# Kernel tuning notes

Hardware: AMD Instinct MI355X
Metric: run time of the kernel (lower is better)

The kernel has to match this reference:

```python
import jax, jax.numpy as jnp
import numpy as np

IB = 8; WB = 8; ABMVM = 8; ABNM = 8; N_MSB = 4; NL = 0.0  # noise_level=0 -> deterministic
B = 4096; IN = 1024; H = 1024

sg = jax.lax.stop_gradient

def quant_raw(x, bits, r):
    step = 2.0 ** (bits - 1)
    xs = jnp.clip(x / r, -1.0 + 1.0 / step, 1.0 - 1.0 / step)
    return jnp.round(xs * step) / step * r

def quant_ste(x, bits, r):
    # straight-through: value = quantized, grad = identity wrt x, no grad to r
    return x + sg(quant_raw(x, bits, r) - x)

def pact(x, a):
    # sign(x)*0.5*(|x| - ||x|-a| + a) == clamp(x, -a, a), kept literal for fidelity
    return jnp.sign(x) * 0.5 * (jnp.abs(x) - jnp.abs(jnp.abs(x) - a) + a)

def bitsplit(x, bits, n_msb):
    # symmetric bit-splitting; STE backward: each y_i has identity grad wrt x
    ste = x - sg(x)
    xv = sg(x)
    beta = 1.0
    ys = []
    for _ in range(n_msb):
        y = quant_raw(xv / beta, bits, 1.0)
        xv = xv - y * beta
        ys.append(y + ste)
        beta = beta / 2.0
    betas = jnp.asarray([1.0 / (2.0 ** i) for i in range(n_msb)], dtype=x.dtype)
    return jnp.stack(ys), betas  # [n_msb, B, D], [n_msb]

def custom_mm(inp, w, b, key):
    # forward: inp @ (quant(clamp(w)) + noise) + quant(b) + noise
    # backward (torch custom): grads use RAW w/b -> STE via out_lin path
    kw, kb = jax.random.split(key)
    n = inp.shape[0]
    noise_w = jax.random.normal(kw, (n, w.shape[1], w.shape[2]), dtype=w.dtype) * NL
    noise_b = jax.random.normal(kb, (n, 1, b.shape[2]), dtype=b.dtype) * NL
    wq = quant_raw(jnp.clip(w, -1.0, 1.0), WB, 1.0)
    bq = quant_raw(b, WB, 1.0)
    out_val = jnp.einsum('nbi,nio->nbo', inp, wq + noise_w) + (bq + noise_b)
    out_lin = jnp.einsum('nbi,io->nbo', inp, w[0]) + b
    return out_lin + sg(out_val - out_lin)

def _cell(input, hx, cx, weight_ih, weight_hh, bias_ih, bias_hh,
          a1, a3, a4, a5, a6, a7, a8, a9, a10, a11):
    k1, k2 = jax.random.split(jax.random.key(42))
    ys, betas = bitsplit(pact(input, a1) / a1, IB, N_MSB)
    out_q = quant_ste(custom_mm(ys, weight_ih, bias_ih, k1), ABMVM, 1.0)
    part1 = (betas[:, None, None] * out_q).sum(0) * a1          # [B, 4H]
    ys, betas = bitsplit(pact(hx, a11) / a11, IB, N_MSB)
    out_q = quant_ste(custom_mm(ys, weight_hh, bias_hh, k2), ABMVM, 1.0)
    part2 = (betas[:, None, None] * out_q).sum(0) * a11
    gates = part1 + part2
    i, j, f, o = jnp.split(gates, 4, axis=1)
    fg = quant_ste(pact(jax.nn.sigmoid(f), a3), ABNM, a3)
    ig = quant_ste(pact(jax.nn.sigmoid(i), a4), ABNM, a4)
    act = quant_ste(pact(jnp.tanh(j), a5), ABNM, a5)
    og = quant_ste(pact(jax.nn.sigmoid(o), a6), ABNM, a6)
    gc = quant_ste(pact(cx * fg, a7), ABNM, a7)
    ai = quant_ste(pact(ig * act, a8), ABNM, a8)
    new_c = quant_ste(pact(gc + ai, a9), ABNM, a9)
    ac = quant_ste(pact(jnp.tanh(new_c), a10), ABNM, a10)
    new_h = quant_ste(pact(ac * og, a11), ABNM, a11)
    return jnp.stack([new_h, new_c])  # [2, B, H]

def setup_inputs() -> dict:
    key = jax.random.key(0)
    ks = jax.random.split(key, 7)
    return {
        'input': jax.random.normal(ks[0], (B, IN), dtype=jnp.float32),
        'hx': jax.random.normal(ks[1], (B, H), dtype=jnp.float32),
        'cx': jax.random.normal(ks[2], (B, H), dtype=jnp.float32),
        'weight_ih': jax.random.normal(ks[3], (1, IN, 4 * H), dtype=jnp.float32) * 0.05,
        'weight_hh': jax.random.normal(ks[4], (1, H, 4 * H), dtype=jnp.float32) * 0.05,
        'bias_ih': jax.random.normal(ks[5], (1, 1, 4 * H), dtype=jnp.float32) * 0.05,
        'bias_hh': jax.random.normal(ks[6], (1, 1, 4 * H), dtype=jnp.float32) * 0.05,
        'a1': jnp.array([128.0]), 'a3': jnp.array([1.0]), 'a4': jnp.array([1.0]),
        'a5': jnp.array([1.0]), 'a6': jnp.array([1.0]), 'a7': jnp.array([4.0]),
        'a8': jnp.array([1.0]), 'a9': jnp.array([4.0]), 'a10': jnp.array([1.0]),
        'a11': jnp.array([4.0]),
    }

def reference(input, hx, cx, weight_ih, weight_hh, bias_ih, bias_hh,
              a1, a3, a4, a5, a6, a7, a8, a9, a10, a11):
    return _cell(input, hx, cx, weight_ih, weight_hh, bias_ih, bias_hh,
                 a1, a3, a4, a5, a6, a7, a8, a9, a10, a11)
```

## Files before the change

kernel.cpp:

```cpp
#include <hip/hip_runtime.h>
#include <cstdint>

typedef unsigned short u16;
typedef __attribute__((ext_vector_type(4))) int i32x4;

#define DEVI __device__ __forceinline__

DEVI float pactf(float x, float a) {
    float ax = fabsf(x);
    float w  = fabsf(ax - a);
    float t  = (ax - w) + a;
    float s  = (x > 0.f) ? 0.5f : ((x < 0.f) ? -0.5f : 0.0f);
    return s * t;
}
DEVI float quantf(float x, float r) {
    float xs = x / r;
    xs = fminf(fmaxf(xs, -0.9921875f), 0.9921875f);
    float e = rintf(xs * 128.0f);
    return (e * 0.0078125f) * r;
}
DEVI float sigf(float x) {
    float eg  = (float)exp(-(double)x);
    float den = 1.0f + eg;
    return 1.0f / den;
}
DEVI float tanf32(float x) { return (float)tanh((double)x); }

#define KSIG  4436
#define NSIG  8873
#define KTANH 2309
#define NTANH 4619

DEVI float sig_lut(float g, const float* __restrict__ Ts) {
    float g256 = g * 256.0f;
    float kf = rintf(g256);
    if (kf == g256) {
        if (kf >  (float)KSIG) return 1.0f;
        if (kf < -(float)KSIG) return 0.0f;
        return Ts[(int)kf + KSIG];
    }
    return sigf(g);
}
DEVI float tanh_lut(float g, const float* __restrict__ Tt) {
    float g256 = g * 256.0f;
    float kf = rintf(g256);
    if (kf == g256) {
        if (fabsf(kf) <= (float)KTANH) return Tt[(int)kf + KTANH];
        return copysignf(1.0f, g);
    }
    return tanf32(g);
}

__global__ void prep_misc(const float* __restrict__ b0, const float* __restrict__ b1,
                          float* __restrict__ Bf, float* __restrict__ Ts,
                          float* __restrict__ Tt) {
    int i = blockIdx.x * 256 + threadIdx.x;
    if (i < NSIG)  Ts[i] = sigf((float)(i - KSIG)  * 0.00390625f);
    if (i < NTANH) Tt[i] = tanf32((float)(i - KTANH) * 0.00390625f);
    if (i < 8192) {
        int proj = i >> 12, nn = i & 4095;
        const float* b = proj ? b1 : b0;
        float v = b[nn];
        float xs = fminf(fmaxf(v, -0.9921875f), 0.9921875f);
        int np_ = ((nn & 1023) << 2) | (nn >> 10);
        Bf[proj * 4096 + np_] = rintf(xs * 128.f);
    }
}

__global__ void prep_act2(const float* __restrict__ X0, const float* __restrict__ X1,
                          const float* __restrict__ a1p, const float* __restrict__ a11p,
                          signed char* __restrict__ A) {
    int blk = blockIdx.x;
    int lo = (blk < 4096) ? 1 : 0;
    const float* X = lo ? X0 : X1;
    float a = lo ? a1p[0] : a11p[0];
    int planebase = lo ? 0 : 4;
    int idx4 = ((blk & 4095) * 256 + threadIdx.x) * 4;
    float4 xv4 = *(const float4*)(X + idx4);
    float v[4] = {xv4.x, xv4.y, xv4.z, xv4.w};
    signed char e4[4][4];
#pragma unroll
    for (int el = 0; el < 4; el++) {
        float x = pactf(v[el], a) / a;
        float xv = x;
        float beta = 1.0f;
#pragma unroll
        for (int n = 0; n < 4; n++) {
            float xs = xv / beta;
            xs = fminf(fmaxf(xs, -0.9921875f), 0.9921875f);
            float e = rintf(xs * 128.0f);
            e4[n][el] = (signed char)(int)e;
            float y = e * 0.0078125f;
            xv = xv - y * beta;
            beta = beta * 0.5f;
        }
    }
#pragma unroll
    for (int n = 0; n < 4; n++)
        *(char4*)(A + (size_t)(planebase + n) * 4194304u + idx4) =
            make_char4(e4[n][0], e4[n][1], e4[n][2], e4[n][3]);
}

__global__ void prep_w(const float* __restrict__ W0, const float* __restrict__ W1,
                       signed char* __restrict__ Wt) {
    __shared__ float tile[32][33];
    int proj = blockIdx.z;
    const float* W = proj ? W1 : W0;
    int n0 = blockIdx.x * 32, k0 = blockIdx.y * 32;
    int tx = threadIdx.x, ty = threadIdx.y;
#pragma unroll
    for (int i = 0; i < 4; i++)
        tile[ty + i * 8][tx] = W[(size_t)(k0 + ty + i * 8) * 4096 + n0 + tx];
    __syncthreads();
#pragma unroll
    for (int i = 0; i < 4; i++) {
        int nn = n0 + ty + i * 8;
        float w = tile[tx][ty + i * 8];
        float xs = fminf(fmaxf(w, -0.9921875f), 0.9921875f);
        float e = rintf(xs * 128.f);
        int np_ = ((nn & 1023) << 2) | (nn >> 10);
        Wt[(size_t)proj * 4194304u + (size_t)np_ * 1024 + k0 + tx] =
            (signed char)(int)e;
    }
}

#define GLOAD16(gp, lp) __builtin_amdgcn_global_load_lds( \
    (const __attribute__((address_space(1))) void*)(gp),  \
    (__attribute__((address_space(3))) void*)(lp), 16, 0, 0)

__global__ __launch_bounds__(512, 4) void gemm_fused(
    const signed char* __restrict__ A, const signed char* __restrict__ Wt,
    const float* __restrict__ Bf, const float* __restrict__ cx,
    float* __restrict__ out,
    const float* __restrict__ Ts, const float* __restrict__ Tt,
    const float* __restrict__ a1p, const float* __restrict__ a3p,
    const float* __restrict__ a4p, const float* __restrict__ a5p,
    const float* __restrict__ a6p, const float* __restrict__ a7p,
    const float* __restrict__ a8p, const float* __restrict__ a9p,
    const float* __restrict__ a10p, const float* __restrict__ a11p) {
    __shared__ __align__(16) signed char lds[67584];
    int tid = threadIdx.x;
    int c0 = blockIdx.x * 128;
    int b0 = blockIdx.y * 128;

    int srow = tid >> 2;
    int g16  = (((tid & 3) + 4 - ((tid >> 3) & 3)) & 3) * 16;
    const signed char* Ab = A + (size_t)(b0 + srow) * 1024 + g16;
    const signed char* Bb = Wt + (size_t)(c0 + srow) * 1024 + g16;

    int w = tid >> 6, l = tid & 63;
    int wm = (w >> 1) * 32, wn = (w & 1) * 64;
    int quad = l >> 4, lrow = l & 15;

    int stoff = tid * 16;
    int slot  = ((quad + (lrow >> 1)) & 3) * 16;
    int fAoff = (wm + lrow) * 64 + slot;
    int fBoff = 8192 + (wn + lrow) * 64 + slot;

    float biasA[4], biasB[4];
#pragma unroll
    for (int nt = 0; nt < 4; nt++) {
        int col = c0 + wn + nt * 16 + lrow;
        biasA[nt] = Bf[col];
        biasB[nt] = Bf[4096 + col];
    }

    i32x4 acc[2][4] = {};
    i32x4 packed[2][4];
#pragma unroll
    for (int mt = 0; mt < 2; mt++)
#pragma unroll
        for (int nt = 0; nt < 4; nt++)
            packed[mt][nt] = (i32x4){0x08000800, 0x08000800, 0x08000800, 0x08000800};

#define STAGE(bufbase, ts)                                              \
    do {                                                                \
        size_t ao = ((size_t)((ts) >> 4) << 22) + (size_t)(((ts) & 15) << 6); \
        size_t bo = (((ts) >= 64) ? (size_t)4194304u : 0) + (size_t)(((ts) & 15) << 6); \
        signed char* lb = lds + (bufbase) + stoff;                      \
        GLOAD16(Ab + ao, lb);                                           \
        GLOAD16(Bb + bo, lb + 8192);                                    \
    } while (0)

#define COMPUTE(bufbase)                                                \
    do {                                                                \
        const signed char* fA = lds + (bufbase) + fAoff;                \
        const signed char* fB = lds + (bufbase) + fBoff;                \
        i32x4 af[2], bfr[4];                                            \
        _Pragma("unroll")                                               \
        for (int mt = 0; mt < 2; mt++) af[mt] = *(const i32x4*)(fA + mt * 1024); \
        _Pragma("unroll")                                               \
        for (int nt = 0; nt < 4; nt++) bfr[nt] = *(const i32x4*)(fB + nt * 1024); \
        _Pragma("unroll")                                               \
        for (int mt = 0; mt < 2; mt++)                                  \
            _Pragma("unroll")                                           \
            for (int nt = 0; nt < 4; nt++)                              \
                acc[mt][nt] = __builtin_amdgcn_mfma_i32_16x16x64_i8(    \
                    af[mt], bfr[nt], acc[mt][nt], 0, 0, 0);             \
    } while (0)

#define FOLD(plane)                                                     \
    do {                                                                \
        int wgt = 8 >> ((plane) & 3);                                   \
        int mulw = ((plane) < 4) ? wgt : (wgt << 16);                   \
        _Pragma("unroll")                                               \
        for (int mt = 0; mt < 2; mt++)                                  \
            _Pragma("unroll")                                           \
            for (int nt = 0; nt < 4; nt++) {                            \
                float bb = ((plane) < 4) ? biasA[nt] : biasB[nt];       \
                _Pragma("unroll")                                       \
                for (int r = 0; r < 4; r++) {                           \
                    float t = (float)acc[mt][nt][r] * 0.0078125f + bb;  \
                    float tc = fminf(fmaxf(t, -127.f), 127.f);          \
                    packed[mt][nt][r] += mulw * (int)rintf(tc);         \
                    acc[mt][nt][r] = 0;                                 \
                }                                                       \
            }                                                           \
    } while (0)

    STAGE(0, 0);
    asm volatile("s_waitcnt vmcnt(0)" ::: "memory");
    __syncthreads();

    for (int it = 0; it < 64; ++it) {
        STAGE(16384, 2 * it + 1);
        COMPUTE(0);
        __syncthreads();
        if (it < 63) STAGE(0, 2 * it + 2);
        COMPUTE(16384);
        if ((it & 7) == 7) FOLD(it >> 3);
        __syncthreads();
    }
#undef STAGE
#undef COMPUTE
#undef FOLD

    float a1v = a1p[0], a11v = a11p[0];
#pragma unroll
    for (int mt = 0; mt < 2; mt++)
#pragma unroll
        for (int nt = 0; nt < 4; nt++)
#pragma unroll
            for (int r = 0; r < 4; r++) {
                int row = wm + mt * 16 + quad * 4 + r;
                int col = wn + nt * 16 + lrow;
                int pk = packed[mt][nt][r];
                int s1 = (pk & 0xFFFF) - 2048;
                int s2 = (pk >> 16) - 2048;
                float gate = ((float)s1 * 0.0009765625f) * a1v +
                             ((float)s2 * 0.0009765625f) * a11v;
                *(float*)(lds + row * 528 + col * 4) = gate;
            }
    __syncthreads();

    float a3 = a3p[0], a4 = a4p[0], a5 = a5p[0], a6 = a6p[0], a7 = a7p[0];
    float a8 = a8p[0], a9 = a9p[0], a10 = a10p[0], a11 = a11p[0];

    int row = tid >> 2;
    int hc  = (tid & 3) * 8;
    size_t obase = (size_t)(b0 + row) * 1024 + (c0 >> 2) + hc;
    float4 cx0 = *(const float4*)(cx + obase);
    float4 cx1 = *(const float4*)(cx + obase + 4);
    float cxa[8] = {cx0.x, cx0.y, cx0.z, cx0.w, cx1.x, cx1.y, cx1.z, cx1.w};
    float nh[8], ncv[8];
#pragma unroll
    for (int j = 0; j < 8; j++) {
        float4 g4 = *(const float4*)(lds + row * 528 + (hc + j) * 16);
        float gi = g4.x, gj = g4.y, gf = g4.z, go = g4.w;
        float fg  = quantf(pactf(sig_lut(gf, Ts), a3), a3);
        float ig  = quantf(pactf(sig_lut(gi, Ts), a4), a4);
        float act = quantf(pactf(tanh_lut(gj, Tt), a5), a5);
        float og  = quantf(pactf(sig_lut(go, Ts), a6), a6);
        float gc  = quantf(pactf(cxa[j] * fg, a7), a7);
        float ai  = quantf(pactf(ig * act, a8), a8);
        float nc  = quantf(pactf(gc + ai, a9), a9);
        float ac  = quantf(pactf(tanh_lut(nc, Tt), a10), a10);
        float hh  = quantf(pactf(ac * og, a11), a11);
        nh[j]  = hh;
        ncv[j] = nc;
    }
    *(float4*)(out + obase)                 = (float4){nh[0], nh[1], nh[2], nh[3]};
    *(float4*)(out + obase + 4)             = (float4){nh[4], nh[5], nh[6], nh[7]};
    *(float4*)(out + 4194304u + obase)      = (float4){ncv[0], ncv[1], ncv[2], ncv[3]};
    *(float4*)(out + 4194304u + obase + 4)  = (float4){ncv[4], ncv[5], ncv[6], ncv[7]};
}

extern "C" void kernel_launch(void* const* d_in, const int* in_sizes, int n_in,
                              void* d_out, int out_size, void* d_ws, size_t ws_size,
                              hipStream_t stream) {
    const float* input = (const float*)d_in[0];
    const float* hx    = (const float*)d_in[1];
    const float* cx    = (const float*)d_in[2];
    const float* wih   = (const float*)d_in[3];
    const float* whh   = (const float*)d_in[4];
    const float* bih   = (const float*)d_in[5];
    const float* bhh   = (const float*)d_in[6];
    const float* a1  = (const float*)d_in[7];
    const float* a3  = (const float*)d_in[8];
    const float* a4  = (const float*)d_in[9];
    const float* a5  = (const float*)d_in[10];
    const float* a6  = (const float*)d_in[11];
    const float* a7  = (const float*)d_in[12];
    const float* a8  = (const float*)d_in[13];
    const float* a9  = (const float*)d_in[14];
    const float* a10 = (const float*)d_in[15];
    const float* a11 = (const float*)d_in[16];

    char* ws = (char*)d_ws;
    signed char* A  = (signed char*)ws;
    signed char* Wt = (signed char*)(ws + 33554432);
    float*       Bf = (float*)(ws + 41943040);
    float*       Ts = (float*)(ws + 41975808);
    float*       Tt = (float*)(ws + 42011300);

    prep_misc<<<35, 256, 0, stream>>>(bih, bhh, Bf, Ts, Tt);
    prep_act2<<<8192, 256, 0, stream>>>(input, hx, a1, a11, A);
    prep_w<<<dim3(128, 32, 2), dim3(32, 8), 0, stream>>>(wih, whh, Wt);
    gemm_fused<<<dim3(32, 32), 512, 0, stream>>>(A, Wt, Bf, cx, (float*)d_out,
                                                 Ts, Tt, a1, a3, a4, a5, a6,
                                                 a7, a8, a9, a10, a11);
}
```

Baseline: 334.7 us.

## Use 256-thread blocks with 64x64 warp tiles and 4-stage LDS pipeline

```diff
diff --git a/kernel.cpp b/kernel.cpp
--- a/kernel.cpp
+++ b/kernel.cpp
@@ -128,7 +128,13 @@
     (const __attribute__((address_space(1))) void*)(gp),  \
     (__attribute__((address_space(3))) void*)(lp), 16, 0, 0)
 
-__global__ __launch_bounds__(512, 4) void gemm_fused(
+#define WB8 asm volatile("s_waitcnt vmcnt(8) lgkmcnt(0)" ::: "memory")
+#define WB4 asm volatile("s_waitcnt vmcnt(4) lgkmcnt(0)" ::: "memory")
+#define WB0 asm volatile("s_waitcnt vmcnt(0) lgkmcnt(0)" ::: "memory")
+#define RAWBAR() do { __builtin_amdgcn_s_barrier(); \
+                      asm volatile("" ::: "memory"); } while (0)
+
+__global__ __launch_bounds__(256, 2) void gemm_fused(
     const signed char* __restrict__ A, const signed char* __restrict__ Wt,
     const float* __restrict__ Bf, const float* __restrict__ cx,
     float* __restrict__ out,
@@ -149,7 +155,7 @@
     const signed char* Bb = Wt + (size_t)(c0 + srow) * 1024 + g16;
 
     int w = tid >> 6, l = tid & 63;
-    int wm = (w >> 1) * 32, wn = (w & 1) * 64;
+    int wm = (w >> 1) * 64, wn = (w & 1) * 64;
     int quad = l >> 4, lrow = l & 15;
 
     int stoff = tid * 16;
@@ -165,10 +171,10 @@
         biasB[nt] = Bf[4096 + col];
     }
 
-    i32x4 acc[2][4] = {};
-    i32x4 packed[2][4];
-#pragma unroll
-    for (int mt = 0; mt < 2; mt++)
+    i32x4 acc[4][4] = {};
+    i32x4 packed[4][4];
+#pragma unroll
+    for (int mt = 0; mt < 4; mt++)
 #pragma unroll
         for (int nt = 0; nt < 4; nt++)
             packed[mt][nt] = (i32x4){0x08000800, 0x08000800, 0x08000800, 0x08000800};
@@ -178,21 +184,23 @@
         size_t ao = ((size_t)((ts) >> 4) << 22) + (size_t)(((ts) & 15) << 6); \
         size_t bo = (((ts) >= 64) ? (size_t)4194304u : 0) + (size_t)(((ts) & 15) << 6); \
         signed char* lb = lds + (bufbase) + stoff;                      \
-        GLOAD16(Ab + ao, lb);                                           \
-        GLOAD16(Bb + bo, lb + 8192);                                    \
+        GLOAD16(Ab + ao,             lb);                               \
+        GLOAD16(Ab + ao + 64 * 1024, lb + 4096);                        \
+        GLOAD16(Bb + bo,             lb + 8192);                        \
+        GLOAD16(Bb + bo + 64 * 1024, lb + 12288);                       \
     } while (0)
 
 #define COMPUTE(bufbase)                                                \
     do {                                                                \
         const signed char* fA = lds + (bufbase) + fAoff;                \
         const signed char* fB = lds + (bufbase) + fBoff;                \
-        i32x4 af[2], bfr[4];                                            \
+        i32x4 af[4], bfr[4];                                            \
         _Pragma("unroll")                                               \
-        for (int mt = 0; mt < 2; mt++) af[mt] = *(const i32x4*)(fA + mt * 1024); \
+        for (int mt = 0; mt < 4; mt++) af[mt] = *(const i32x4*)(fA + mt * 1024); \
         _Pragma("unroll")                                               \
         for (int nt = 0; nt < 4; nt++) bfr[nt] = *(const i32x4*)(fB + nt * 1024); \
         _Pragma("unroll")                                               \
-        for (int mt = 0; mt < 2; mt++)                                  \
+        for (int mt = 0; mt < 4; mt++)                                  \
             _Pragma("unroll")                                           \
             for (int nt = 0; nt < 4; nt++)                              \
                 acc[mt][nt] = __builtin_amdgcn_mfma_i32_16x16x64_i8(    \
@@ -201,13 +209,14 @@
 
 #define FOLD(plane)                                                     \
     do {                                                                \
-        int wgt = 8 >> ((plane) & 3);                                   \
-        int mulw = ((plane) < 4) ? wgt : (wgt << 16);                   \
+        int pl = (plane);                                               \
+        int wgt = 8 >> (pl & 3);                                        \
+        int mulw = (pl < 4) ? wgt : (wgt << 16);                        \
         _Pragma("unroll")                                               \
-        for (int mt = 0; mt < 2; mt++)                                  \
+        for (int mt = 0; mt < 4; mt++)                                  \
             _Pragma("unroll")                                           \
             for (int nt = 0; nt < 4; nt++) {                            \
-                float bb = ((plane) < 4) ? biasA[nt] : biasB[nt];       \
+                float bb = (pl < 4) ? biasA[nt] : biasB[nt];            \
                 _Pragma("unroll")                                       \
                 for (int r = 0; r < 4; r++) {                           \
                     float t = (float)acc[mt][nt][r] * 0.0078125f + bb;  \
@@ -219,25 +228,29 @@
     } while (0)
 
     STAGE(0, 0);
-    asm volatile("s_waitcnt vmcnt(0)" ::: "memory");
-    __syncthreads();
-
-    for (int it = 0; it < 64; ++it) {
-        STAGE(16384, 2 * it + 1);
-        COMPUTE(0);
-        __syncthreads();
-        if (it < 63) STAGE(0, 2 * it + 2);
-        COMPUTE(16384);
-        if ((it & 7) == 7) FOLD(it >> 3);
-        __syncthreads();
-    }
+    STAGE(16384, 1);
+    STAGE(32768, 2);
+
+    for (int tb = 0; tb < 124; tb += 4) {
+        WB8; RAWBAR(); STAGE(49152, tb + 3); COMPUTE(0);
+        WB8; RAWBAR(); STAGE(0,     tb + 4); COMPUTE(16384);
+        WB8; RAWBAR(); STAGE(16384, tb + 5); COMPUTE(32768);
+        WB8; RAWBAR(); STAGE(32768, tb + 6); COMPUTE(49152);
+        if ((tb & 15) == 12) FOLD((tb + 3) >> 4);
+    }
+    WB8; RAWBAR(); STAGE(49152, 127); COMPUTE(0);
+    WB8; RAWBAR(); COMPUTE(16384);
+    WB4; RAWBAR(); COMPUTE(32768);
+    WB0; RAWBAR(); COMPUTE(49152);
+    FOLD(7);
 #undef STAGE
 #undef COMPUTE
 #undef FOLD
 
+    __syncthreads();
     float a1v = a1p[0], a11v = a11p[0];
 #pragma unroll
-    for (int mt = 0; mt < 2; mt++)
+    for (int mt = 0; mt < 4; mt++)
 #pragma unroll
         for (int nt = 0; nt < 4; nt++)
 #pragma unroll
@@ -256,15 +269,18 @@
     float a3 = a3p[0], a4 = a4p[0], a5 = a5p[0], a6 = a6p[0], a7 = a7p[0];
     float a8 = a8p[0], a9 = a9p[0], a10 = a10p[0], a11 = a11p[0];
 
-    int row = tid >> 2;
-    int hc  = (tid & 3) * 8;
+    int row = tid >> 1;
+    int hc  = (tid & 1) * 16;
     size_t obase = (size_t)(b0 + row) * 1024 + (c0 >> 2) + hc;
-    float4 cx0 = *(const float4*)(cx + obase);
-    float4 cx1 = *(const float4*)(cx + obase + 4);
-    float cxa[8] = {cx0.x, cx0.y, cx0.z, cx0.w, cx1.x, cx1.y, cx1.z, cx1.w};
-    float nh[8], ncv[8];
-#pragma unroll
-    for (int j = 0; j < 8; j++) {
+    float cxa[16], nh[16], ncv[16];
+#pragma unroll
+    for (int q = 0; q < 4; q++) {
+        float4 c4 = *(const float4*)(cx + obase + q * 4);
+        cxa[q * 4] = c4.x; cxa[q * 4 + 1] = c4.y;
+        cxa[q * 4 + 2] = c4.z; cxa[q * 4 + 3] = c4.w;
+    }
+#pragma unroll
+    for (int j = 0; j < 16; j++) {
         float4 g4 = *(const float4*)(lds + row * 528 + (hc + j) * 16);
         float gi = g4.x, gj = g4.y, gf = g4.z, go = g4.w;
         float fg  = quantf(pactf(sig_lut(gf, Ts), a3), a3);
@@ -279,10 +295,13 @@
         nh[j]  = hh;
         ncv[j] = nc;
     }
-    *(float4*)(out + obase)                 = (float4){nh[0], nh[1], nh[2], nh[3]};
-    *(float4*)(out + obase + 4)             = (float4){nh[4], nh[5], nh[6], nh[7]};
-    *(float4*)(out + 4194304u + obase)      = (float4){ncv[0], ncv[1], ncv[2], ncv[3]};
-    *(float4*)(out + 4194304u + obase + 4)  = (float4){ncv[4], ncv[5], ncv[6], ncv[7]};
+#pragma unroll
+    for (int q = 0; q < 4; q++) {
+        *(float4*)(out + obase + q * 4) =
+            (float4){nh[q * 4], nh[q * 4 + 1], nh[q * 4 + 2], nh[q * 4 + 3]};
+        *(float4*)(out + 4194304u + obase + q * 4) =
+            (float4){ncv[q * 4], ncv[q * 4 + 1], ncv[q * 4 + 2], ncv[q * 4 + 3]};
+    }
 }
 
 extern "C" void kernel_launch(void* const* d_in, const int* in_sizes, int n_in,
@@ -316,7 +335,7 @@
     prep_misc<<<35, 256, 0, stream>>>(bih, bhh, Bf, Ts, Tt);
     prep_act2<<<8192, 256, 0, stream>>>(input, hx, a1, a11, A);
     prep_w<<<dim3(128, 32, 2), dim3(32, 8), 0, stream>>>(wih, whh, Wt);
-    gemm_fused<<<dim3(32, 32), 512, 0, stream>>>(A, Wt, Bf, cx, (float*)d_out,
+    gemm_fused<<<dim3(32, 32), 256, 0, stream>>>(A, Wt, Bf, cx, (float*)d_out,
                                                  Ts, Tt, a1, a3, a4, a5, a6,
                                                  a7, a8, a9, a10, a11);
 }
```

Result: slower. 353.4 us (+5.6%).
